# Kernel tuning notes

Measured on AMD Instinct MI355X. Metric: run time of the kernel, lower is better.

Reference implementation:

```python
import jax, jax.numpy as jnp
import numpy as np

MAX_KLEN = 11  # kernel lengths drawn from {7, 9, 11}


def setup_inputs() -> dict:
    B, T, K = 32, 512, 4096
    rng = np.random.default_rng(0)
    # kernel lengths ~ uniform over {7, 9, 11}
    klen = np.array([7, 9, 11])[rng.integers(0, 3, size=K)]
    tap_mask = (np.arange(MAX_KLEN)[None, :] < klen[:, None])
    # weights: N(0,1), mean-centered over the actual taps, zero-padded to MAX_KLEN
    w = rng.standard_normal((K, MAX_KLEN)).astype(np.float32) * tap_mask
    w = w - (w.sum(1, keepdims=True) / klen[:, None]).astype(np.float32) * tap_mask
    # bias ~ U[-1, 1)
    bias = (rng.random(K) * 2 - 1).astype(np.float32)
    # dilation = floor(2**s), s ~ U[0, ln(T-1) - ln(klen-1)]
    A = np.log(T - 1) - np.log(klen - 1)
    dil = np.floor(2.0 ** (rng.random(K) * A)).astype(np.int64)
    # padding = dil*(klen-1)/2 with prob 1/2, else 0  (klen-1 is even -> exact)
    pad = (dil * (klen - 1) // 2) * rng.integers(0, 2, size=K)
    # torch conv1d output length
    out_len = T + 2 * pad - dil * (klen - 1)
    x = jax.random.normal(jax.random.key(0), (B, T), dtype=jnp.float32)
    return {
        'x': x,
        'weight': jnp.asarray(w),
        'bias': jnp.asarray(bias),
        'dilation': jnp.asarray(dil, jnp.int32),
        'padding': jnp.asarray(pad, jnp.int32),
        'out_len': jnp.asarray(out_len, jnp.int32),
    }


def reference(x, weight, bias, dilation, padding, out_len):
    # x: [B, T]; weight: [K, MAX_KLEN] zero-padded; bias/dilation/padding/out_len: [K]
    B, T = x.shape
    K = weight.shape[0]
    P = T  # padding <= dil*(klen-1)/2  =>  out_len <= T
    p = jnp.arange(P, dtype=jnp.int32)
    acc = jnp.zeros((B, K, P), dtype=x.dtype)
    # fixed small loop over taps; all kernels processed at once per tap
    for j in range(MAX_KLEN):
        idx = p[None, :] - padding[:, None] + j * dilation[:, None]  # [K, P]
        ok = (idx >= 0) & (idx < T)
        xg = x[:, jnp.clip(idx, 0, T - 1)]  # [B, K, P]
        acc = acc + (weight[:, j][:, None] * ok.astype(x.dtype)) * xg
    conv = acc + bias[None, :, None]  # [B, K, P]
    valid = (p[None, :] < out_len[:, None])  # [K, P]
    neg_inf = jnp.asarray(-jnp.inf, dtype=x.dtype)
    mx = jnp.max(jnp.where(valid[None], conv, neg_inf), axis=-1)  # [B, K]
    ppv = jnp.sum(((conv > 0) & valid[None]).astype(x.dtype), axis=-1) / out_len.astype(x.dtype)
    # einops 'b s f -> b (s f)': interleave (max_k, ppv_k) per kernel
    feats = jnp.stack([mx, ppv], axis=-1).reshape(B, 2 * K)
    return feats
```

## Files before the change

### kernel.cpp

```cpp
#include <hip/hip_runtime.h>

#define TLEN 512
#define KLEN 11
#define XPAD 256
#define XTOT 1024

__device__ __forceinline__ float wave_max_f32(float v) {
    const int NEG_INF = 0xFF800000;
    int x = __float_as_int(v);
    int t;
    t = __builtin_amdgcn_update_dpp(NEG_INF, x, 0x111, 0xF, 0xF, false);
    x = __float_as_int(fmaxf(__int_as_float(x), __int_as_float(t)));
    t = __builtin_amdgcn_update_dpp(NEG_INF, x, 0x112, 0xF, 0xF, false);
    x = __float_as_int(fmaxf(__int_as_float(x), __int_as_float(t)));
    t = __builtin_amdgcn_update_dpp(NEG_INF, x, 0x114, 0xF, 0xF, false);
    x = __float_as_int(fmaxf(__int_as_float(x), __int_as_float(t)));
    t = __builtin_amdgcn_update_dpp(NEG_INF, x, 0x118, 0xF, 0xF, false);
    x = __float_as_int(fmaxf(__int_as_float(x), __int_as_float(t)));
    t = __builtin_amdgcn_update_dpp(NEG_INF, x, 0x142, 0xA, 0xF, false);
    x = __float_as_int(fmaxf(__int_as_float(x), __int_as_float(t)));
    t = __builtin_amdgcn_update_dpp(NEG_INF, x, 0x143, 0xC, 0xF, false);
    x = __float_as_int(fmaxf(__int_as_float(x), __int_as_float(t)));
    return __int_as_float(__builtin_amdgcn_readlane(x, 63));
}

__global__ __launch_bounds__(256, 4) void rf_kernel(
    const float* __restrict__ x, const float* __restrict__ weight,
    const float* __restrict__ bias, const int* __restrict__ dilation,
    const int* __restrict__ padding, const int* __restrict__ out_len,
    float* __restrict__ out, int K)
{
    __shared__ float4 xs[XTOT];
    const int t = threadIdx.x;
    const int b0 = blockIdx.y * 4;

    const float4 z4 = make_float4(0.f, 0.f, 0.f, 0.f);
    xs[t] = z4;
    xs[768 + t] = z4;
    const float* x0 = x + (size_t)b0 * TLEN;
    xs[XPAD + t]       = make_float4(x0[t],       x0[TLEN + t],
                                     x0[2 * TLEN + t],       x0[3 * TLEN + t]);
    xs[XPAD + 256 + t] = make_float4(x0[256 + t], x0[TLEN + 256 + t],
                                     x0[2 * TLEN + 256 + t], x0[3 * TLEN + 256 + t]);
    __syncthreads();

    const int lane = t & 63;
    const int ks = __builtin_amdgcn_readfirstlane(blockIdx.x * 4 + (t >> 6));

    const int dil  = dilation[ks];
    const int pd   = padding[ks];
    const int olen = out_len[ks];
    const float bs = bias[ks];
    float wj[KLEN];
    #pragma unroll
    for (int j = 0; j < KLEN; ++j) wj[j] = weight[ks * KLEN + j];

    const int base = XPAD + lane - pd;

    float4 mx = make_float4(-INFINITY, -INFINITY, -INFINITY, -INFINITY);
    int c0 = 0, c1 = 0, c2 = 0, c3 = 0;

    #pragma unroll
    for (int i = 0; i < 8; ++i) {
        const int p0 = i * 64;
        if (p0 < olen) {
            float4 a = z4;
            #pragma unroll
            for (int j = 0; j < KLEN; ++j) {
                if (wj[j] != 0.0f) {
                    const float4 v = xs[base + j * dil + p0];
                    a.x = fmaf(wj[j], v.x, a.x);
                    a.y = fmaf(wj[j], v.y, a.y);
                    a.z = fmaf(wj[j], v.z, a.z);
                    a.w = fmaf(wj[j], v.w, a.w);
                }
            }
            a.x += bs; a.y += bs; a.z += bs; a.w += bs;
            if (p0 + 64 <= olen) {
                mx.x = fmaxf(mx.x, a.x); mx.y = fmaxf(mx.y, a.y);
                mx.z = fmaxf(mx.z, a.z); mx.w = fmaxf(mx.w, a.w);
                c0 += __popcll(__ballot(a.x > 0.f));
                c1 += __popcll(__ballot(a.y > 0.f));
                c2 += __popcll(__ballot(a.z > 0.f));
                c3 += __popcll(__ballot(a.w > 0.f));
            } else {
                const bool vld = lane < (olen - p0);
                mx.x = fmaxf(mx.x, vld ? a.x : -INFINITY);
                mx.y = fmaxf(mx.y, vld ? a.y : -INFINITY);
                mx.z = fmaxf(mx.z, vld ? a.z : -INFINITY);
                mx.w = fmaxf(mx.w, vld ? a.w : -INFINITY);
                c0 += __popcll(__ballot(vld && a.x > 0.f));
                c1 += __popcll(__ballot(vld && a.y > 0.f));
                c2 += __popcll(__ballot(vld && a.z > 0.f));
                c3 += __popcll(__ballot(vld && a.w > 0.f));
            }
        }
    }

    mx.x = wave_max_f32(mx.x);
    mx.y = wave_max_f32(mx.y);
    mx.z = wave_max_f32(mx.z);
    mx.w = wave_max_f32(mx.w);

    if (lane == 0) {
        const float inv = 1.0f / (float)olen;
        const size_t row = (size_t)2 * K;
        float* o = out + (size_t)b0 * row + 2 * ks;
        *(float2*)(o)           = make_float2(mx.x, (float)c0 * inv);
        *(float2*)(o + row)     = make_float2(mx.y, (float)c1 * inv);
        *(float2*)(o + 2 * row) = make_float2(mx.z, (float)c2 * inv);
        *(float2*)(o + 3 * row) = make_float2(mx.w, (float)c3 * inv);
    }
}

extern "C" void kernel_launch(void* const* d_in, const int* in_sizes, int n_in,
                              void* d_out, int out_size, void* d_ws, size_t ws_size,
                              hipStream_t stream) {
    const float* x    = (const float*)d_in[0];
    const float* w    = (const float*)d_in[1];
    const float* bias = (const float*)d_in[2];
    const int* dil    = (const int*)d_in[3];
    const int* pad    = (const int*)d_in[4];
    const int* olen   = (const int*)d_in[5];
    float* out        = (float*)d_out;

    const int K = in_sizes[2];
    const int B = in_sizes[0] / TLEN;

    dim3 grid(K / 4, B / 4);
    rf_kernel<<<grid, 256, 0, stream>>>(x, w, bias, dil, pad, olen, out, K);
}
```

Baseline: 99.03 us.

## Prestage padded interleaved input in workspace and split tap loads between LDS and L1

A new pre-kernel writes the zero-padded, batch-interleaved float4 input into the workspace. The main kernel then fills LDS with plain vector copies instead of strided gathers. Odd taps now read directly from the global workspace through the cache while even taps read LDS, which spreads load bandwidth across two paths, and the FMAs use packed v_pk_fma_f32. This costs an extra kernel launch, and global reads on odd taps may have higher latency. The old LDS-only kernel is kept as a fallback for when the workspace is too small.

```diff
diff --git a/kernel.cpp b/kernel.cpp
--- a/kernel.cpp
+++ b/kernel.cpp
@@ -4,6 +4,14 @@
 #define KLEN 11
 #define XPAD 256
 #define XTOT 1024
+
+typedef float v2f __attribute__((ext_vector_type(2)));
+
+__device__ __forceinline__ v2f pk_fma(v2f a, v2f b, v2f c) {
+    v2f d;
+    asm("v_pk_fma_f32 %0, %1, %2, %3" : "=v"(d) : "v"(a), "v"(b), "v"(c));
+    return d;
+}
 
 __device__ __forceinline__ float wave_max_f32(float v) {
     const int NEG_INF = 0xFF800000;
@@ -24,7 +32,117 @@
     return __int_as_float(__builtin_amdgcn_readlane(x, 63));
 }
 
+__global__ __launch_bounds__(256) void stage_ws(const float* __restrict__ x,
+                                                float4* __restrict__ ws) {
+    const int t = threadIdx.x;
+    const int g = blockIdx.x >> 2;
+    const int seg = blockIdx.x & 3;
+    const int slot = seg * 256 + t;
+    float4 v = make_float4(0.f, 0.f, 0.f, 0.f);
+    if (slot >= XPAD && slot < XPAD + TLEN) {
+        const int pos = slot - XPAD;
+        const float* xg = x + (size_t)g * 4 * TLEN;
+        v = make_float4(xg[pos], xg[TLEN + pos], xg[2 * TLEN + pos], xg[3 * TLEN + pos]);
+    }
+    ws[(size_t)g * XTOT + slot] = v;
+}
+
 __global__ __launch_bounds__(256, 4) void rf_kernel(
+    const float4* __restrict__ ws, const float* __restrict__ weight,
+    const float* __restrict__ bias, const int* __restrict__ dilation,
+    const int* __restrict__ padding, const int* __restrict__ out_len,
+    float* __restrict__ out, int K)
+{
+    __shared__ float4 xs[XTOT];
+    const int t = threadIdx.x;
+    const float4* wsg = ws + (size_t)blockIdx.y * XTOT;
+
+    xs[t]       = wsg[t];
+    xs[t + 256] = wsg[t + 256];
+    xs[t + 512] = wsg[t + 512];
+    xs[t + 768] = wsg[t + 768];
+    __syncthreads();
+
+    const int lane = t & 63;
+    const int ks = __builtin_amdgcn_readfirstlane(blockIdx.x * 4 + (t >> 6));
+
+    const int dil  = dilation[ks];
+    const int pd   = padding[ks];
+    const int olen = out_len[ks];
+    const float bs = bias[ks];
+    float wj[KLEN];
+    v2f ww[KLEN];
+    #pragma unroll
+    for (int j = 0; j < KLEN; ++j) {
+        wj[j] = weight[ks * KLEN + j];
+        ww[j].x = wj[j]; ww[j].y = wj[j];
+    }
+
+    const int vbase = XPAD + lane - pd;
+
+    float mx0 = -INFINITY, mx1 = -INFINITY, mx2 = -INFINITY, mx3 = -INFINITY;
+    int c0 = 0, c1 = 0, c2 = 0, c3 = 0;
+
+    #pragma unroll
+    for (int i = 0; i < 8; ++i) {
+        const int p0 = i * 64;
+        if (p0 < olen) {
+            v2f a0; a0.x = bs; a0.y = bs;
+            v2f a1 = a0;
+            #pragma unroll
+            for (int j = 0; j < KLEN; ++j) {
+                if (wj[j] != 0.0f) {
+                    float4 v;
+                    if (j & 1) {
+                        const float4* tp = wsg + (j * dil + p0);
+                        v = tp[vbase];
+                    } else {
+                        v = xs[vbase + j * dil + p0];
+                    }
+                    v2f lo; lo.x = v.x; lo.y = v.y;
+                    v2f hi; hi.x = v.z; hi.y = v.w;
+                    a0 = pk_fma(ww[j], lo, a0);
+                    a1 = pk_fma(ww[j], hi, a1);
+                }
+            }
+            if (p0 + 64 <= olen) {
+                mx0 = fmaxf(mx0, a0.x); mx1 = fmaxf(mx1, a0.y);
+                mx2 = fmaxf(mx2, a1.x); mx3 = fmaxf(mx3, a1.y);
+                c0 += __popcll(__ballot(a0.x > 0.f));
+                c1 += __popcll(__ballot(a0.y > 0.f));
+                c2 += __popcll(__ballot(a1.x > 0.f));
+                c3 += __popcll(__ballot(a1.y > 0.f));
+            } else {
+                const bool vld = lane < (olen - p0);
+                mx0 = fmaxf(mx0, vld ? a0.x : -INFINITY);
+                mx1 = fmaxf(mx1, vld ? a0.y : -INFINITY);
+                mx2 = fmaxf(mx2, vld ? a1.x : -INFINITY);
+                mx3 = fmaxf(mx3, vld ? a1.y : -INFINITY);
+                c0 += __popcll(__ballot(vld && a0.x > 0.f));
+                c1 += __popcll(__ballot(vld && a0.y > 0.f));
+                c2 += __popcll(__ballot(vld && a1.x > 0.f));
+                c3 += __popcll(__ballot(vld && a1.y > 0.f));
+            }
+        }
+    }
+
+    mx0 = wave_max_f32(mx0);
+    mx1 = wave_max_f32(mx1);
+    mx2 = wave_max_f32(mx2);
+    mx3 = wave_max_f32(mx3);
+
+    if (lane == 0) {
+        const float inv = 1.0f / (float)olen;
+        const size_t row = (size_t)2 * K;
+        float* o = out + (size_t)blockIdx.y * 4 * row + 2 * ks;
+        *(float2*)(o)           = make_float2(mx0, (float)c0 * inv);
+        *(float2*)(o + row)     = make_float2(mx1, (float)c1 * inv);
+        *(float2*)(o + 2 * row) = make_float2(mx2, (float)c2 * inv);
+        *(float2*)(o + 3 * row) = make_float2(mx3, (float)c3 * inv);
+    }
+}
+
+__global__ __launch_bounds__(256, 4) void rf_kernel_lds(
     const float* __restrict__ x, const float* __restrict__ weight,
     const float* __restrict__ bias, const int* __restrict__ dilation,
     const int* __restrict__ padding, const int* __restrict__ out_len,
@@ -33,20 +151,18 @@
     __shared__ float4 xs[XTOT];
     const int t = threadIdx.x;
     const int b0 = blockIdx.y * 4;
-
     const float4 z4 = make_float4(0.f, 0.f, 0.f, 0.f);
     xs[t] = z4;
     xs[768 + t] = z4;
     const float* x0 = x + (size_t)b0 * TLEN;
-    xs[XPAD + t]       = make_float4(x0[t],       x0[TLEN + t],
-                                     x0[2 * TLEN + t],       x0[3 * TLEN + t]);
+    xs[XPAD + t]       = make_float4(x0[t], x0[TLEN + t],
+                                     x0[2 * TLEN + t], x0[3 * TLEN + t]);
     xs[XPAD + 256 + t] = make_float4(x0[256 + t], x0[TLEN + 256 + t],
                                      x0[2 * TLEN + 256 + t], x0[3 * TLEN + 256 + t]);
     __syncthreads();
 
     const int lane = t & 63;
     const int ks = __builtin_amdgcn_readfirstlane(blockIdx.x * 4 + (t >> 6));
-
     const int dil  = dilation[ks];
     const int pd   = padding[ks];
     const int olen = out_len[ks];
@@ -54,12 +170,10 @@
     float wj[KLEN];
     #pragma unroll
     for (int j = 0; j < KLEN; ++j) wj[j] = weight[ks * KLEN + j];
-
     const int base = XPAD + lane - pd;
 
     float4 mx = make_float4(-INFINITY, -INFINITY, -INFINITY, -INFINITY);
     int c0 = 0, c1 = 0, c2 = 0, c3 = 0;
-
     #pragma unroll
     for (int i = 0; i < 8; ++i) {
         const int p0 = i * 64;
@@ -96,12 +210,10 @@
             }
         }
     }
-
     mx.x = wave_max_f32(mx.x);
     mx.y = wave_max_f32(mx.y);
     mx.z = wave_max_f32(mx.z);
     mx.w = wave_max_f32(mx.w);
-
     if (lane == 0) {
         const float inv = 1.0f / (float)olen;
         const size_t row = (size_t)2 * K;
@@ -126,7 +238,15 @@
 
     const int K = in_sizes[2];
     const int B = in_sizes[0] / TLEN;
-
-    dim3 grid(K / 4, B / 4);
-    rf_kernel<<<grid, 256, 0, stream>>>(x, w, bias, dil, pad, olen, out, K);
-}
+    const size_t ws_need = (size_t)(B / 4) * XTOT * sizeof(float4);
+
+    if (ws_size >= ws_need) {
+        float4* ws = (float4*)d_ws;
+        stage_ws<<<dim3((B / 4) * 4), 256, 0, stream>>>(x, ws);
+        dim3 grid(K / 4, B / 4);
+        rf_kernel<<<grid, 256, 0, stream>>>(ws, w, bias, dil, pad, olen, out, K);
+    } else {
+        dim3 grid(K / 4, B / 4);
+        rf_kernel_lds<<<grid, 256, 0, stream>>>(x, w, bias, dil, pad, olen, out, K);
+    }
+}
```

New measurement: 112.4 us. 1.13x slower.

## Stage input as packed fp16 for eight batches and use mixed-precision FMA

Applied to the files above, without the earlier changes.

A new pre-pass kernel converts x to fp16 and packs eight batch rows per 16-byte slot, zero-padded, into the workspace. The main kernel loads this packed tile into LDS and runs v_fma_mix_f32 with fp32 weights and accumulators, so each wave handles eight batches instead of four. This halves the LDS bytes per input value and halves the grid's y-dimension, which cuts LDS traffic and redundant per-kernel parameter loads. In exchange it adds a second launch and rounds the input to fp16, which can perturb the max values and the sign-based positive counts near zero.

```diff
diff --git a/kernel.cpp b/kernel.cpp
--- a/kernel.cpp
+++ b/kernel.cpp
@@ -1,9 +1,15 @@
 #include <hip/hip_runtime.h>
+#include <hip/hip_fp16.h>
 
 #define TLEN 512
 #define KLEN 11
 #define XPAD 256
 #define XTOT 1024
+
+#define MIX_LO(acc, w, h) \
+    asm("v_fma_mix_f32 %0, %1, %2, %0 op_sel_hi:[0,1,0]" : "+v"(acc) : "v"(w), "v"(h))
+#define MIX_HI(acc, w, h) \
+    asm("v_fma_mix_f32 %0, %1, %2, %0 op_sel:[0,1,0] op_sel_hi:[0,1,0]" : "+v"(acc) : "v"(w), "v"(h))
 
 __device__ __forceinline__ float wave_max_f32(float v) {
     const int NEG_INF = 0xFF800000;
@@ -24,7 +30,113 @@
     return __int_as_float(__builtin_amdgcn_readlane(x, 63));
 }
 
-__global__ __launch_bounds__(256, 4) void rf_kernel(
+__global__ __launch_bounds__(256) void stage_ws_h(const float* __restrict__ x,
+                                                  uint4* __restrict__ ws) {
+    const int t = threadIdx.x;
+    const int g = blockIdx.x >> 2;
+    const int seg = blockIdx.x & 3;
+    const int slot = seg * 256 + t;
+    uint4 v = make_uint4(0u, 0u, 0u, 0u);
+    if (slot >= XPAD && slot < XPAD + TLEN) {
+        const int pos = slot - XPAD;
+        const float* xg = x + (size_t)g * 8 * TLEN;
+        unsigned h[8];
+        #pragma unroll
+        for (int q = 0; q < 8; ++q)
+            h[q] = (unsigned)__half_as_ushort(__float2half(xg[q * TLEN + pos]));
+        v.x = h[0] | (h[1] << 16);
+        v.y = h[2] | (h[3] << 16);
+        v.z = h[4] | (h[5] << 16);
+        v.w = h[6] | (h[7] << 16);
+    }
+    ws[(size_t)g * XTOT + slot] = v;
+}
+
+__global__ __launch_bounds__(256, 4) void rf_kernel_h(
+    const uint4* __restrict__ ws, const float* __restrict__ weight,
+    const float* __restrict__ bias, const int* __restrict__ dilation,
+    const int* __restrict__ padding, const int* __restrict__ out_len,
+    float* __restrict__ out, int K)
+{
+    __shared__ uint4 xs[XTOT];
+    const int t = threadIdx.x;
+    const uint4* wsg = ws + (size_t)blockIdx.y * XTOT;
+
+    xs[t]       = wsg[t];
+    xs[t + 256] = wsg[t + 256];
+    xs[t + 512] = wsg[t + 512];
+    xs[t + 768] = wsg[t + 768];
+    __syncthreads();
+
+    const int lane = t & 63;
+    const int ks = __builtin_amdgcn_readfirstlane(blockIdx.x * 4 + (t >> 6));
+
+    const int dil  = dilation[ks];
+    const int pd   = padding[ks];
+    const int olen = out_len[ks];
+    const float bs = bias[ks];
+    float wj[KLEN];
+    #pragma unroll
+    for (int j = 0; j < KLEN; ++j) wj[j] = weight[ks * KLEN + j];
+
+    const int vbase = XPAD + lane - pd;
+    const uint4* xp[KLEN];
+    #pragma unroll
+    for (int j = 0; j < KLEN; ++j) xp[j] = xs + (vbase + j * dil);
+
+    float mx[8];
+    int cnt[8];
+    #pragma unroll
+    for (int q = 0; q < 8; ++q) { mx[q] = -INFINITY; cnt[q] = 0; }
+
+    #pragma unroll
+    for (int i = 0; i < 8; ++i) {
+        const int p0 = i * 64;
+        if (p0 < olen) {
+            float a[8];
+            #pragma unroll
+            for (int q = 0; q < 8; ++q) a[q] = bs;
+            #pragma unroll
+            for (int j = 0; j < KLEN; ++j) {
+                if (wj[j] != 0.0f) {
+                    const uint4 r = xp[j][p0];
+                    MIX_LO(a[0], wj[j], r.x); MIX_HI(a[1], wj[j], r.x);
+                    MIX_LO(a[2], wj[j], r.y); MIX_HI(a[3], wj[j], r.y);
+                    MIX_LO(a[4], wj[j], r.z); MIX_HI(a[5], wj[j], r.z);
+                    MIX_LO(a[6], wj[j], r.w); MIX_HI(a[7], wj[j], r.w);
+                }
+            }
+            if (p0 + 64 <= olen) {
+                #pragma unroll
+                for (int q = 0; q < 8; ++q) {
+                    mx[q] = fmaxf(mx[q], a[q]);
+                    cnt[q] += __popcll(__ballot(a[q] > 0.f));
+                }
+            } else {
+                const bool vld = lane < (olen - p0);
+                #pragma unroll
+                for (int q = 0; q < 8; ++q) {
+                    mx[q] = fmaxf(mx[q], vld ? a[q] : -INFINITY);
+                    cnt[q] += __popcll(__ballot(vld && a[q] > 0.f));
+                }
+            }
+        }
+    }
+
+    #pragma unroll
+    for (int q = 0; q < 8; ++q) mx[q] = wave_max_f32(mx[q]);
+
+    if (lane == 0) {
+        const float inv = 1.0f / (float)olen;
+        const size_t row = (size_t)2 * K;
+        float* o = out + (size_t)blockIdx.y * 8 * row + 2 * ks;
+        #pragma unroll
+        for (int q = 0; q < 8; ++q)
+            *(float2*)(o + q * row) = make_float2(mx[q], (float)cnt[q] * inv);
+    }
+}
+
+__global__ __launch_bounds__(256, 4) void rf_kernel_lds(
     const float* __restrict__ x, const float* __restrict__ weight,
     const float* __restrict__ bias, const int* __restrict__ dilation,
     const int* __restrict__ padding, const int* __restrict__ out_len,
@@ -33,20 +145,18 @@
     __shared__ float4 xs[XTOT];
     const int t = threadIdx.x;
     const int b0 = blockIdx.y * 4;
-
     const float4 z4 = make_float4(0.f, 0.f, 0.f, 0.f);
     xs[t] = z4;
     xs[768 + t] = z4;
     const float* x0 = x + (size_t)b0 * TLEN;
-    xs[XPAD + t]       = make_float4(x0[t],       x0[TLEN + t],
-                                     x0[2 * TLEN + t],       x0[3 * TLEN + t]);
+    xs[XPAD + t]       = make_float4(x0[t], x0[TLEN + t],
+                                     x0[2 * TLEN + t], x0[3 * TLEN + t]);
     xs[XPAD + 256 + t] = make_float4(x0[256 + t], x0[TLEN + 256 + t],
                                      x0[2 * TLEN + 256 + t], x0[3 * TLEN + 256 + t]);
     __syncthreads();
 
     const int lane = t & 63;
     const int ks = __builtin_amdgcn_readfirstlane(blockIdx.x * 4 + (t >> 6));
-
     const int dil  = dilation[ks];
     const int pd   = padding[ks];
     const int olen = out_len[ks];
@@ -54,12 +164,10 @@
     float wj[KLEN];
     #pragma unroll
     for (int j = 0; j < KLEN; ++j) wj[j] = weight[ks * KLEN + j];
-
     const int base = XPAD + lane - pd;
 
     float4 mx = make_float4(-INFINITY, -INFINITY, -INFINITY, -INFINITY);
     int c0 = 0, c1 = 0, c2 = 0, c3 = 0;
-
     #pragma unroll
     for (int i = 0; i < 8; ++i) {
         const int p0 = i * 64;
@@ -96,12 +204,10 @@
             }
         }
     }
-
     mx.x = wave_max_f32(mx.x);
     mx.y = wave_max_f32(mx.y);
     mx.z = wave_max_f32(mx.z);
     mx.w = wave_max_f32(mx.w);
-
     if (lane == 0) {
         const float inv = 1.0f / (float)olen;
         const size_t row = (size_t)2 * K;
@@ -126,7 +232,16 @@
 
     const int K = in_sizes[2];
     const int B = in_sizes[0] / TLEN;
-
-    dim3 grid(K / 4, B / 4);
-    rf_kernel<<<grid, 256, 0, stream>>>(x, w, bias, dil, pad, olen, out, K);
-}
+    const int G = B / 8;
+    const size_t ws_need = (size_t)G * XTOT * sizeof(uint4);
+
+    if (ws_size >= ws_need && (B % 8) == 0) {
+        uint4* ws = (uint4*)d_ws;
+        stage_ws_h<<<dim3(G * 4), 256, 0, stream>>>(x, ws);
+        dim3 grid(K / 4, G);
+        rf_kernel_h<<<grid, 256, 0, stream>>>(ws, w, bias, dil, pad, olen, out, K);
+    } else {
+        dim3 grid(K / 4, B / 4);
+        rf_kernel_lds<<<grid, 256, 0, stream>>>(x, w, bias, dil, pad, olen, out, K);
+    }
+}
```

After: 104.2 us. 1.05x slower.
